# Optimization experiments

Measured on AMD Instinct MI355X. Metric: run time of the kernel, lower is better.

## Reference

```python
import jax, jax.numpy as jnp
import numpy as np

NUM_HEADS = 16
NUM_GROUPS = 4
HEAD_DIM = 128  # d_out // num_heads


def setup_inputs() -> dict:
    key = jax.random.key(0)
    ks = jax.random.split(key, 6)
    b, t, d_in, d_out = 4, 2048, 2048, 2048
    kv_dim = NUM_GROUPS * HEAD_DIM
    s = 0.02
    return {
        "x": jax.random.normal(ks[0], (b, t, d_in), jnp.float32),
        "Wq": jax.random.normal(ks[1], (d_in, d_out), jnp.float32) * s,
        "Wk": jax.random.normal(ks[2], (d_in, kv_dim), jnp.float32) * s,
        "Wv": jax.random.normal(ks[3], (d_in, kv_dim), jnp.float32) * s,
        "Wo": jax.random.normal(ks[4], (d_out, d_out), jnp.float32) * s,
        "bo": jnp.zeros((d_out,), jnp.float32),
    }


def reference(x, Wq, Wk, Wv, Wo, bo):
    b, t, _ = x.shape
    H, G, D = NUM_HEADS, NUM_GROUPS, HEAD_DIM
    P = H // G  # heads_per_group
    # Projections
    q = (x @ Wq).reshape(b, t, G, P, D)          # head h = g*P + p matches repeat_interleave
    k = (x @ Wk).reshape(b, t, G, D)
    v = (x @ Wv).reshape(b, t, G, D)
    # Scores: [b, G, P, tq, tk] (grouped form of repeat_interleave over heads)
    scores = jnp.einsum('bqgpd,bkgd->bgpqk', q, k)
    # Causal mask: q_pos < k_pos -> -inf
    qpos = jnp.arange(t)
    mask = qpos[:, None] < qpos[None, :]  # [tq, tk], True above diagonal
    scores = jnp.where(mask[None, None, None], -jnp.inf, scores)
    attn = jax.nn.softmax(scores / np.float32(np.sqrt(D)), axis=-1)
    ctx = jnp.einsum('bgpqk,bkgd->bqgpd', attn, v)  # [b, t, G, P, D]
    ctx = ctx.reshape(b, t, H * D)
    return ctx @ Wo + bo
```

## Files before the change

kernel.cpp:

```cpp
#include <hip/hip_runtime.h>
#include <hip/hip_bf16.h>
#include <stdint.h>
#include <math.h>

#define T_SEQ 2048
#define D_MODEL 2048
#define KV_DIM 512
#define QKV_LD 3072
#define NHEADS 16
#define HDIM 128
#define BATCH 4
#define MT (BATCH * T_SEQ)

typedef __attribute__((ext_vector_type(4))) float f32x4;
typedef __attribute__((ext_vector_type(8))) __bf16 bf16x8;
typedef __attribute__((ext_vector_type(4))) __bf16 bf16x4;
typedef __attribute__((ext_vector_type(8))) unsigned short u16x8;
typedef __attribute__((ext_vector_type(4))) unsigned short u16x4;
typedef __attribute__((ext_vector_type(4))) short s16x4;

static __device__ __forceinline__ unsigned short f32_bf16(float f) {
  unsigned u = __float_as_uint(f);
  u += 0x7fff + ((u >> 16) & 1);
  return (unsigned short)(u >> 16);
}

static __device__ __forceinline__ void gload_lds16(const void* g, void* l) {
  __builtin_amdgcn_global_load_lds(
      (__attribute__((address_space(1))) void*)(const_cast<void*>(g)),
      (__attribute__((address_space(3))) void*)l, 16, 0, 0);
}

static __device__ __forceinline__ f32x4 mfma16(bf16x8 a, bf16x8 b, f32x4 c) {
  return __builtin_amdgcn_mfma_f32_16x16x32_bf16(a, b, c, 0, 0, 0);
}

static __device__ __forceinline__ f32x4 mfma16x16(u16x4 a, u16x4 b, f32x4 c) {
#if __has_builtin(__builtin_amdgcn_mfma_f32_16x16x16bf16_1k)
  return __builtin_amdgcn_mfma_f32_16x16x16bf16_1k(
      __builtin_bit_cast(s16x4, a), __builtin_bit_cast(s16x4, b), c, 0, 0, 0);
#elif __has_builtin(__builtin_amdgcn_mfma_f32_16x16x16_bf16)
  return __builtin_amdgcn_mfma_f32_16x16x16_bf16(
      __builtin_bit_cast(bf16x4, a), __builtin_bit_cast(bf16x4, b), c, 0, 0, 0);
#else
  f32x4 d;
  asm("v_mfma_f32_16x16x16_bf16 %0, %1, %2, %3" : "=v"(d) : "v"(a), "v"(b), "v"(c));
  return d;
#endif
}

static __device__ __forceinline__ void barx() {
  asm volatile("" ::: "memory");
  __builtin_amdgcn_s_barrier();
  asm volatile("" ::: "memory");
}

#define VIDX(d, c) (((((d) << 3) + ((c) ^ ((d) & 7))) << 3))

__global__ void cvt_kernel(const float* __restrict__ in, unsigned short* __restrict__ out, int n4) {
  int i = blockIdx.x * 256 + threadIdx.x;
  if (i >= n4) return;
  f32x4 v = ((const f32x4*)in)[i];
  u16x4 o;
#pragma unroll
  for (int j = 0; j < 4; ++j) o[j] = f32_bf16(v[j]);
  ((u16x4*)out)[i] = o;
}

__global__ void transpose_kernel(const float* __restrict__ W, unsigned short* __restrict__ Wt,
                                 int K, int N) {
  __shared__ float tile[32][33];
  int bx = blockIdx.x * 32;
  int by = blockIdx.y * 32;
  int tx = threadIdx.x, ty = threadIdx.y;
#pragma unroll
  for (int i = 0; i < 32; i += 8)
    tile[ty + i][tx] = W[(size_t)(by + ty + i) * N + bx + tx];
  __syncthreads();
#pragma unroll
  for (int i = 0; i < 32; i += 8)
    Wt[(size_t)(bx + ty + i) * K + by + tx] = f32_bf16(tile[tx][ty + i]);
}

template <typename OutT, bool HAS_BIAS>
__global__ __launch_bounds__(512, 2) void gemm256_kernel(
    const unsigned short* __restrict__ A, const unsigned short* __restrict__ Bt,
    OutT* __restrict__ C, const float* __restrict__ bias, int M, int N, int K) {
  __shared__ unsigned short As[2][16384];
  __shared__ unsigned short Bs[2][16384];
  const int tid = threadIdx.x;
  const int wave = tid >> 6, lane = tid & 63;
  const int lr = lane & 15, lh = lane >> 4;
  const int wm = wave >> 2, wn = wave & 3;

  const int gx = gridDim.x;
  const int nwg = gx * gridDim.y;
  int flat = blockIdx.y * gx + blockIdx.x;
  flat = (flat & 7) * (nwg >> 3) + (flat >> 3);
  const int bx = flat % gx, by = flat / gx;

  const unsigned short* Ag = A + (size_t)by * 256 * K;
  const unsigned short* Bg = Bt + (size_t)bx * 256 * K;

  const int srow_lo = lane >> 2;
  const int sbcol = ((lane & 3) * 16) ^ ((srow_lo & 8) << 2);
  const int scol = sbcol >> 1;

#define STAGE_HALF(SRC, DST, HK)                                            \
  {                                                                         \
    _Pragma("unroll") for (int s = 0; s < 2; ++s) {                         \
      const int jj = s * 8 + wave;                                          \
      gload_lds16((SRC) + (size_t)(jj * 16 + srow_lo) * K + (HK) * 32 + scol, \
                  (char*)(DST) + (jj * 2 + (HK)) * 1024);                   \
    }                                                                       \
  }

  const int aoff = lr * 32 + ((lh * 8) ^ ((lr & 8) << 1));
  const int abase = wm * 8 * 1024;
  const int bbase = wn * 4 * 1024;

  f32x4 acc[8][4] = {};
  bf16x8 af[4], bf[4];

#define PH_READ_A(MH, KS)                                                   \
  {                                                                         \
    _Pragma("unroll") for (int m = 0; m < 4; ++m)                           \
      af[m] = *(const bf16x8*)&As[cur][abase + ((MH)*4 + m) * 1024 + (KS)*512 + aoff]; \
  }
#define PH_READ_B(KS)                                                       \
  {                                                                         \
    _Pragma("unroll") for (int n = 0; n < 4; ++n)                           \
      bf[n] = *(const bf16x8*)&Bs[cur][bbase + n * 1024 + (KS)*512 + aoff]; \
  }
#define PH_MFMA(MH)                                                         \
  {                                                                         \
    __builtin_amdgcn_s_setprio(1);                                          \
    _Pragma("unroll") for (int m = 0; m < 4; ++m)                           \
      _Pragma("unroll") for (int n = 0; n < 4; ++n)                         \
        acc[(MH)*4 + m][n] = mfma16(af[m], bf[n], acc[(MH)*4 + m][n]);      \
    __builtin_amdgcn_s_setprio(0);                                          \
  }

  STAGE_HALF(Ag, As[0], 0);
  STAGE_HALF(Bg, Bs[0], 0);
  STAGE_HALF(Ag, As[0], 1);
  STAGE_HALF(Bg, Bs[0], 1);
  asm volatile("s_waitcnt vmcnt(4)" ::: "memory");
  barx();

  const int NT = K >> 6;
  for (int t = 0; t < NT; ++t) {
    const int cur = t & 1;
    const bool pf = (t + 1 < NT);
    const unsigned short* An = Ag + (size_t)(t + 1) * 64;
    const unsigned short* Bn = Bg + (size_t)(t + 1) * 64;
    unsigned short* Ad = As[cur ^ 1];
    unsigned short* Bd = Bs[cur ^ 1];

    PH_READ_A(0, 0); PH_READ_B(0);
    if (pf) STAGE_HALF(An, Ad, 0);
    barx(); PH_MFMA(0); barx();

    PH_READ_A(1, 0);
    if (pf) {
      STAGE_HALF(Bn, Bd, 0);
      asm volatile("s_waitcnt vmcnt(4)" ::: "memory");
    } else {
      asm volatile("s_waitcnt vmcnt(0)" ::: "memory");
    }
    barx(); PH_MFMA(1); barx();

    PH_READ_A(0, 1); PH_READ_B(1);
    if (pf) STAGE_HALF(An, Ad, 1);
    barx(); PH_MFMA(0); barx();

    PH_READ_A(1, 1);
    if (pf) {
      STAGE_HALF(Bn, Bd, 1);
      asm volatile("s_waitcnt vmcnt(4)" ::: "memory");
    }
    barx(); PH_MFMA(1); barx();
  }

#pragma unroll
  for (int m8 = 0; m8 < 8; ++m8) {
#pragma unroll
    for (int n = 0; n < 4; ++n) {
      const size_t col = (size_t)bx * 256 + wn * 64 + n * 16 + lr;
      float bv = 0.0f;
      if constexpr (HAS_BIAS) bv = bias[col];
#pragma unroll
      for (int r = 0; r < 4; ++r) {
        const size_t row = (size_t)by * 256 + wm * 128 + m8 * 16 + lh * 4 + r;
        const float val = acc[m8][n][r] + bv;
        if constexpr (sizeof(OutT) == 2)
          ((unsigned short*)C)[row * N + col] = f32_bf16(val);
        else
          ((float*)C)[row * N + col] = val;
      }
    }
  }
#undef STAGE_HALF
#undef PH_READ_A
#undef PH_READ_B
#undef PH_MFMA
}

static __device__ __forceinline__ void softmax_step(
    const f32x4 st[4], u16x4 pr[4], float& m_run, float& l_run,
    f32x4* oaccq, bool maskT, int kv0, int qglob, int lh) {
  float p[4][4];
#pragma unroll
  for (int n = 0; n < 4; ++n)
#pragma unroll
    for (int r = 0; r < 4; ++r) {
      float val = st[n][r];
      if (maskT && (kv0 + n * 16 + lh * 4 + r > qglob)) val = -1e30f;
      p[n][r] = val;
    }
  float pm[4];
#pragma unroll
  for (int n = 0; n < 4; ++n)
    pm[n] = fmaxf(fmaxf(p[n][0], p[n][1]), fmaxf(p[n][2], p[n][3]));
  float pmax = fmaxf(fmaxf(pm[0], pm[1]), fmaxf(pm[2], pm[3]));
  pmax = fmaxf(pmax, __shfl_xor(pmax, 16));
  pmax = fmaxf(pmax, __shfl_xor(pmax, 32));
  const bool resc = __any(pmax > m_run + 8.0f);
  float alpha = 1.0f;
  if (resc) {
    const float mnew = fmaxf(m_run, pmax);
    alpha = exp2f(m_run - mnew);
    m_run = mnew;
  }
  float rsum = 0.0f;
#pragma unroll
  for (int n = 0; n < 4; ++n) {
#pragma unroll
    for (int r = 0; r < 4; ++r) {
      p[n][r] = exp2f(p[n][r] - m_run);
      rsum += p[n][r];
    }
    __hip_bfloat162 t0 = __float22bfloat162_rn(make_float2(p[n][0], p[n][1]));
    __hip_bfloat162 t1 = __float22bfloat162_rn(make_float2(p[n][2], p[n][3]));
    unsigned lo, hi;
    __builtin_memcpy(&lo, &t0, 4);
    __builtin_memcpy(&hi, &t1, 4);
    unsigned long long both = (unsigned long long)lo | ((unsigned long long)hi << 32);
    u16x4 pk;
    __builtin_memcpy(&pk, &both, 8);
    pr[n] = pk;
  }
  rsum += __shfl_xor(rsum, 16);
  rsum += __shfl_xor(rsum, 32);
  if (resc) {
    l_run = l_run * alpha + rsum;
#pragma unroll
    for (int r = 0; r < 4; ++r) {
      const float a = __shfl(alpha, lh * 4 + r);
#pragma unroll
      for (int nd = 0; nd < 8; ++nd) oaccq[nd][r] *= a;
    }
  } else {
    l_run += rsum;
  }
}

__global__ __launch_bounds__(256, 2) void attn_kernel(
    const unsigned short* __restrict__ qkv, unsigned short* __restrict__ ctx) {
  const int lin = blockIdx.x;
  const int xcd = lin & 7;
  const int j = lin >> 3;
  const int sel = j & 1;
  const int i = j >> 1;
  const int p = i & 3;
  const int qt = 15 - (i >> 2);
  const int s = xcd * 2 + sel;
  const int b = s >> 2, g = s & 3;
  const int h = g * 4 + p;
  const int tid = threadIdx.x;
  const int wave = tid >> 6, lane = tid & 63;
  const int lr = lane & 15, lh = lane >> 4;
  const int qb = qt * 128;
  const int qrow0 = qb + wave * 16;
  const int qrow1 = qb + 64 + wave * 16;

  __shared__ unsigned short Ks[64 * 128];
  __shared__ unsigned short Vts[128 * 64];

  const int vr0 = (tid & 31) * 2;
  const int vc0 = (tid >> 5) * 16;
  const int vcu = vr0 >> 3, vcw = vr0 & 7;

  const unsigned short* qrow_base = qkv + (size_t)b * T_SEQ * QKV_LD;
  const unsigned short* kbase = qrow_base + D_MODEL + g * HDIM;
  const unsigned short* vbase = qrow_base + D_MODEL + KV_DIM + g * HDIM;

  const float QS = 0.1275174f;
  bf16x8 aq[2][4];
  {
    const unsigned short* qp0 = qrow_base + (size_t)(qrow0 + lr) * QKV_LD + h * HDIM + lh * 8;
    const unsigned short* qp1 = qrow_base + (size_t)(qrow1 + lr) * QKV_LD + h * HDIM + lh * 8;
#pragma unroll
    for (int kk = 0; kk < 4; ++kk) {
      u16x8 r0 = *(const u16x8*)(qp0 + kk * 32);
      u16x8 r1 = *(const u16x8*)(qp1 + kk * 32);
      u16x8 o0, o1;
#pragma unroll
      for (int jj = 0; jj < 8; ++jj) {
        o0[jj] = f32_bf16(__uint_as_float((unsigned)r0[jj] << 16) * QS);
        o1[jj] = f32_bf16(__uint_as_float((unsigned)r1[jj] << 16) * QS);
      }
      aq[0][kk] = __builtin_bit_cast(bf16x8, o0);
      aq[1][kk] = __builtin_bit_cast(bf16x8, o1);
    }
  }

  f32x4 oacc[2][8] = {};
  float m_run0 = -1e30f, l_run0 = 0.0f, m_run1 = -1e30f, l_run1 = 0.0f;

  const int nt = 2 * qt + 2;

  for (int t = 0; t < nt; ++t) {
    const int kv0 = t * 64;
    __syncthreads();
#pragma unroll
    for (int is = 0; is < 4; ++is) {
      const int c = is * 4 + wave;
      const int u = c * 64 + lane;
      const int vu = u ^ ((u >> 4) & 7);
      const int r = vu >> 4;
      const int cc = (vu & 15) * 8;
      gload_lds16(kbase + (size_t)(kv0 + r) * QKV_LD + cc, (char*)Ks + c * 1024);
    }
    {
      const unsigned short* vp = vbase + (size_t)(kv0 + vr0) * QKV_LD + vc0;
      u16x8 va0 = *(const u16x8*)(vp);
      u16x8 va1 = *(const u16x8*)(vp + 8);
      u16x8 vb0 = *(const u16x8*)(vp + QKV_LD);
      u16x8 vb1 = *(const u16x8*)(vp + QKV_LD + 8);
#pragma unroll
      for (int jj = 0; jj < 8; ++jj) {
        const int d0 = vc0 + jj, d1 = vc0 + 8 + jj;
        *(unsigned int*)&Vts[VIDX(d0, vcu) + vcw] =
            (unsigned int)va0[jj] | ((unsigned int)vb0[jj] << 16);
        *(unsigned int*)&Vts[VIDX(d1, vcu) + vcw] =
            (unsigned int)va1[jj] | ((unsigned int)vb1[jj] << 16);
      }
    }
    __syncthreads();

    const bool live0 = (t < nt - 1);
    const bool mask0 = (t == nt - 2);
    const bool mask1 = (t == nt - 1);

    f32x4 st0[4] = {}, st1[4] = {};
    __builtin_amdgcn_s_setprio(1);
#pragma unroll
    for (int n = 0; n < 4; ++n) {
      const int rr = n * 16 + lr;
#pragma unroll
      for (int kk = 0; kk < 4; ++kk) {
        const int lu = rr * 16 + kk * 4 + lh;
        const int pu = lu ^ (rr & 7);
        const bf16x8 ak = *(const bf16x8*)((const char*)Ks + pu * 16);
        if (live0) st0[n] = mfma16(ak, aq[0][kk], st0[n]);
        st1[n] = mfma16(ak, aq[1][kk], st1[n]);
      }
    }
    __builtin_amdgcn_s_setprio(0);

    u16x4 pr0[4], pr1[4];
    if (live0)
      softmax_step(st0, pr0, m_run0, l_run0, oacc[0], mask0, kv0, qrow0 + lr, lh);
    softmax_step(st1, pr1, m_run1, l_run1, oacc[1], mask1, kv0, qrow1 + lr, lh);

    __builtin_amdgcn_s_setprio(1);
#pragma unroll
    for (int n = 0; n < 4; ++n) {
      const int cb = n * 2 + (lh >> 1);
      const int off = (lh & 1) * 4;
#pragma unroll
      for (int nd = 0; nd < 8; ++nd) {
        const int d = nd * 16 + lr;
        const u16x4 vf = *(const u16x4*)&Vts[VIDX(d, cb) + off];
        if (live0) oacc[0][nd] = mfma16x16(pr0[n], vf, oacc[0][nd]);
        oacc[1][nd] = mfma16x16(pr1[n], vf, oacc[1][nd]);
      }
    }
    __builtin_amdgcn_s_setprio(0);
  }

#pragma unroll
  for (int m = 0; m < 2; ++m) {
    const float lm = (m == 0) ? l_run0 : l_run1;
    const int qrow = (m == 0) ? qrow0 : qrow1;
    unsigned short* cp = ctx + ((size_t)b * T_SEQ + qrow) * D_MODEL + h * HDIM;
#pragma unroll
    for (int r = 0; r < 4; ++r) {
      const float inv = 1.0f / __shfl(lm, lh * 4 + r);
#pragma unroll
      for (int nd = 0; nd < 8; ++nd)
        cp[(size_t)(lh * 4 + r) * D_MODEL + nd * 16 + lr] =
            f32_bf16(oacc[m][nd][r] * inv);
    }
  }
}

extern "C" void kernel_launch(void* const* d_in, const int* in_sizes, int n_in,
                              void* d_out, int out_size, void* d_ws, size_t ws_size,
                              hipStream_t stream) {
  const float* x = (const float*)d_in[0];
  const float* Wq = (const float*)d_in[1];
  const float* Wk = (const float*)d_in[2];
  const float* Wv = (const float*)d_in[3];
  const float* Wo = (const float*)d_in[4];
  const float* bo = (const float*)d_in[5];
  float* out = (float*)d_out;

  char* ws = (char*)d_ws;
  unsigned short* xb = (unsigned short*)(ws + 0);
  unsigned short* ctx = (unsigned short*)(ws + 0);
  unsigned short* qkv = (unsigned short*)(ws + 33554432);
  unsigned short* WqkvT = (unsigned short*)(ws + 83886080);
  unsigned short* WoT = (unsigned short*)(ws + 96468992);

  const int n4 = MT * D_MODEL / 4;
  cvt_kernel<<<(n4 + 255) / 256, 256, 0, stream>>>(x, xb, n4);
  dim3 tb(32, 8);
  transpose_kernel<<<dim3(D_MODEL / 32, D_MODEL / 32), tb, 0, stream>>>(
      Wq, WqkvT, D_MODEL, D_MODEL);
  transpose_kernel<<<dim3(KV_DIM / 32, D_MODEL / 32), tb, 0, stream>>>(
      Wk, WqkvT + (size_t)D_MODEL * D_MODEL, D_MODEL, KV_DIM);
  transpose_kernel<<<dim3(KV_DIM / 32, D_MODEL / 32), tb, 0, stream>>>(
      Wv, WqkvT + (size_t)(D_MODEL + KV_DIM) * D_MODEL, D_MODEL, KV_DIM);
  transpose_kernel<<<dim3(D_MODEL / 32, D_MODEL / 32), tb, 0, stream>>>(
      Wo, WoT, D_MODEL, D_MODEL);

  gemm256_kernel<unsigned short, false><<<dim3(QKV_LD / 256, MT / 256), 512, 0, stream>>>(
      xb, WqkvT, qkv, nullptr, MT, QKV_LD, D_MODEL);

  attn_kernel<<<1024, 256, 0, stream>>>(qkv, ctx);

  gemm256_kernel<float, true><<<dim3(D_MODEL / 256, MT / 256), 512, 0, stream>>>(
      ctx, WoT, out, bo, MT, D_MODEL, D_MODEL);
}
```

Baseline: 399.5 us.

## Double-buffer K/V tiles in attention to overlap loads with compute

Allocates two LDS buffers for K and transposed V and issues the next tile's async K loads and V register loads before computing on the current tile. The V transpose-write goes into the alternate buffer after the PV MFMAs, which leaves one barrier per iteration. This aims to hide global memory latency behind the MFMA work. In exchange LDS use doubles to 64KB, the launch-bounds occupancy hint drops from 2 to 1, and the V values held in registers raise register pressure.

```diff
diff --git a/kernel.cpp b/kernel.cpp
--- a/kernel.cpp
+++ b/kernel.cpp
@@ -265,7 +265,7 @@
   }
 }
 
-__global__ __launch_bounds__(256, 2) void attn_kernel(
+__global__ __launch_bounds__(256) void attn_kernel(
     const unsigned short* __restrict__ qkv, unsigned short* __restrict__ ctx) {
   const int lin = blockIdx.x;
   const int xcd = lin & 7;
@@ -284,8 +284,8 @@
   const int qrow0 = qb + wave * 16;
   const int qrow1 = qb + 64 + wave * 16;
 
-  __shared__ unsigned short Ks[64 * 128];
-  __shared__ unsigned short Vts[128 * 64];
+  __shared__ unsigned short Ks[2][64 * 128];
+  __shared__ unsigned short Vts[2][128 * 64];
 
   const int vr0 = (tid & 31) * 2;
   const int vc0 = (tid >> 5) * 16;
@@ -320,39 +320,61 @@
 
   const int nt = 2 * qt + 2;
 
+#define STAGE_K(T, BUF)                                                      \
+  {                                                                          \
+    const int kv0s = (T) * 64;                                               \
+    _Pragma("unroll") for (int is = 0; is < 4; ++is) {                       \
+      const int c = is * 4 + wave;                                           \
+      const int u = c * 64 + lane;                                           \
+      const int vu = u ^ ((u >> 4) & 7);                                     \
+      const int r = vu >> 4;                                                 \
+      const int cc = (vu & 15) * 8;                                          \
+      gload_lds16(kbase + (size_t)(kv0s + r) * QKV_LD + cc,                  \
+                  (char*)(BUF) + c * 1024);                                  \
+    }                                                                        \
+  }
+
+#define LOAD_V(T)                                                               \
+  {                                                                             \
+    const unsigned short* vp = vbase + (size_t)((T) * 64 + vr0) * QKV_LD + vc0; \
+    va0 = *(const u16x8*)(vp);                                                  \
+    va1 = *(const u16x8*)(vp + 8);                                              \
+    vb0 = *(const u16x8*)(vp + QKV_LD);                                         \
+    vb1 = *(const u16x8*)(vp + QKV_LD + 8);                                     \
+  }
+
+#define WRITE_V(BUF)                                                         \
+  {                                                                          \
+    unsigned short* Vb = (BUF);                                              \
+    _Pragma("unroll") for (int jj = 0; jj < 8; ++jj) {                       \
+      const int d0 = vc0 + jj, d1 = vc0 + 8 + jj;                            \
+      *(unsigned int*)&Vb[VIDX(d0, vcu) + vcw] =                             \
+          (unsigned int)va0[jj] | ((unsigned int)vb0[jj] << 16);             \
+      *(unsigned int*)&Vb[VIDX(d1, vcu) + vcw] =                             \
+          (unsigned int)va1[jj] | ((unsigned int)vb1[jj] << 16);             \
+    }                                                                        \
+  }
+
+  u16x8 va0, va1, vb0, vb1;
+  STAGE_K(0, Ks[0]);
+  LOAD_V(0);
+  WRITE_V(Vts[0]);
+  __syncthreads();
+
   for (int t = 0; t < nt; ++t) {
+    const int cur = t & 1;
     const int kv0 = t * 64;
-    __syncthreads();
-#pragma unroll
-    for (int is = 0; is < 4; ++is) {
-      const int c = is * 4 + wave;
-      const int u = c * 64 + lane;
-      const int vu = u ^ ((u >> 4) & 7);
-      const int r = vu >> 4;
-      const int cc = (vu & 15) * 8;
-      gload_lds16(kbase + (size_t)(kv0 + r) * QKV_LD + cc, (char*)Ks + c * 1024);
-    }
-    {
-      const unsigned short* vp = vbase + (size_t)(kv0 + vr0) * QKV_LD + vc0;
-      u16x8 va0 = *(const u16x8*)(vp);
-      u16x8 va1 = *(const u16x8*)(vp + 8);
-      u16x8 vb0 = *(const u16x8*)(vp + QKV_LD);
-      u16x8 vb1 = *(const u16x8*)(vp + QKV_LD + 8);
-#pragma unroll
-      for (int jj = 0; jj < 8; ++jj) {
-        const int d0 = vc0 + jj, d1 = vc0 + 8 + jj;
-        *(unsigned int*)&Vts[VIDX(d0, vcu) + vcw] =
-            (unsigned int)va0[jj] | ((unsigned int)vb0[jj] << 16);
-        *(unsigned int*)&Vts[VIDX(d1, vcu) + vcw] =
-            (unsigned int)va1[jj] | ((unsigned int)vb1[jj] << 16);
-      }
-    }
-    __syncthreads();
+    const bool has_next = (t + 1 < nt);
+    if (has_next) {
+      STAGE_K(t + 1, Ks[cur ^ 1]);
+      LOAD_V(t + 1);
+    }
 
     const bool live0 = (t < nt - 1);
     const bool mask0 = (t == nt - 2);
     const bool mask1 = (t == nt - 1);
 
+    const unsigned short* Kc = Ks[cur];
     f32x4 st0[4] = {}, st1[4] = {};
     __builtin_amdgcn_s_setprio(1);
 #pragma unroll
@@ -362,7 +384,7 @@
       for (int kk = 0; kk < 4; ++kk) {
         const int lu = rr * 16 + kk * 4 + lh;
         const int pu = lu ^ (rr & 7);
-        const bf16x8 ak = *(const bf16x8*)((const char*)Ks + pu * 16);
+        const bf16x8 ak = *(const bf16x8*)((const char*)Kc + pu * 16);
         if (live0) st0[n] = mfma16(ak, aq[0][kk], st0[n]);
         st1[n] = mfma16(ak, aq[1][kk], st1[n]);
       }
@@ -374,6 +396,7 @@
       softmax_step(st0, pr0, m_run0, l_run0, oacc[0], mask0, kv0, qrow0 + lr, lh);
     softmax_step(st1, pr1, m_run1, l_run1, oacc[1], mask1, kv0, qrow1 + lr, lh);
 
+    const unsigned short* Vc = Vts[cur];
     __builtin_amdgcn_s_setprio(1);
 #pragma unroll
     for (int n = 0; n < 4; ++n) {
@@ -382,12 +405,15 @@
 #pragma unroll
       for (int nd = 0; nd < 8; ++nd) {
         const int d = nd * 16 + lr;
-        const u16x4 vf = *(const u16x4*)&Vts[VIDX(d, cb) + off];
+        const u16x4 vf = *(const u16x4*)&Vc[VIDX(d, cb) + off];
         if (live0) oacc[0][nd] = mfma16x16(pr0[n], vf, oacc[0][nd]);
         oacc[1][nd] = mfma16x16(pr1[n], vf, oacc[1][nd]);
       }
     }
     __builtin_amdgcn_s_setprio(0);
+
+    if (has_next) WRITE_V(Vts[cur ^ 1]);
+    __syncthreads();
   }
 
 #pragma unroll
@@ -404,6 +430,9 @@
             f32_bf16(oacc[m][nd][r] * inv);
     }
   }
+#undef STAGE_K
+#undef LOAD_V
+#undef WRITE_V
 }
 
 extern "C" void kernel_launch(void* const* d_in, const int* in_sizes, int n_in,
```

After: 520.5 us. +30.3%, slower.
